# Kernel optimization log

Hardware: AMD Instinct MI355X
Metric: run time of the kernel (lower is better)

Reference implementation:

```python
import jax, jax.numpy as jnp
import numpy as np

B, C, H, W = 8, 64, 112, 112
O, K, PAD, STRIDE = 64, 3, 1, 1
KK = K * K
OH = (H - K + 2 * PAD) // STRIDE + 1
OW = (W - K + 2 * PAD) // STRIDE + 1
L = OH * OW  # number of patches


def setup_inputs() -> dict:
    key = jax.random.key(0)
    k1, k2, k3 = jax.random.split(key, 3)
    x = jax.random.normal(k1, (B, C, H, W), dtype=jnp.float32)
    weight = jax.random.normal(k2, (O, C, K, K), dtype=jnp.float32)
    # one uniformly random kernel position to zero out, per patch (nums=1)
    mask_idx = jax.random.randint(k3, (L,), 0, KK, dtype=jnp.int32)
    return {"x": x, "weight": weight, "mask_idx": mask_idx}


def reference(x, weight, mask_idx):
    b = x.shape[0]
    # im2col: [b, C*KK, OH, OW], feature dim ordered channel-major (c, kh, kw)
    # which matches torch.nn.Unfold ordering.
    patches = jax.lax.conv_general_dilated_patches(
        x, (K, K), (STRIDE, STRIDE), ((PAD, PAD), (PAD, PAD)))
    patches = patches.reshape(b, C * KK, L)  # [b, CK, L]

    # Per-patch mask over kernel positions, tiled across channels
    # (equivalent to mask.repeat(1, in_channels) in the original).
    mask = jnp.ones((L, KK), dtype=x.dtype).at[jnp.arange(L), mask_idx].set(0.0)
    mask_full = jnp.tile(mask, (1, C))  # [L, C*KK]

    # weight.view(O, -1).t() -> [CK, O]; masking the weight rows per patch is
    # mathematically identical to masking the unfolded input per patch, which
    # avoids materializing the [L, CK, O] masked weight tensor.
    w2 = weight.reshape(O, C * KK).T  # [CK, O]
    out = jnp.einsum('bkl,lk,ko->bol', patches, mask_full, w2)  # [b, O, L]
    return out.reshape(b, O, OH, OW)
```

## Files before the change

### kernel.cpp

```cpp
#include <hip/hip_runtime.h>
#include <hip/hip_bf16.h>
#include <cstdint>

#define Bn 8
#define Cn 64
#define Hn 112
#define Wn 112
#define On 64
#define Ln (Hn * Wn)
#define HP 114
#define WP 114

typedef __attribute__((ext_vector_type(4)))  float f32x4;
typedef __attribute__((ext_vector_type(16))) float f32x16;
typedef __attribute__((ext_vector_type(8)))  short bf16x8;
typedef __attribute__((ext_vector_type(4)))  unsigned int u32x4;

__device__ __forceinline__ unsigned f2bf(float f) {
    unsigned u = __float_as_uint(f);
    unsigned r = 0x7fffu + ((u >> 16) & 1u);
    return (u + r) >> 16;
}

__global__ __launch_bounds__(128) void prep_kernel(const float* __restrict__ x,
                                                   const float* __restrict__ w,
                                                   unsigned short* __restrict__ xps,
                                                   unsigned short* __restrict__ wpk) {
    int blk = blockIdx.x;
    int t = threadIdx.x;
    if (blk < 912) {
        int b = blk / HP, row = blk - b * HP;
        int c8  = t >> 4;
        int wpl = t & 15;
        int h = row - 1;
        const float* xb = x + (size_t)b * Cn * Hn * Wn;
        unsigned short* dst = xps + ((size_t)(b * HP + row) * WP) * Cn;
#pragma unroll
        for (int g = 0; g < 8; ++g) {
            int wp = wpl + (g << 4);
            if (wp < WP) {
                int wcol = wp - 1;
                bool inb = ((unsigned)h < (unsigned)Hn) & ((unsigned)wcol < (unsigned)Wn);
                const float* s = xb + ((size_t)(c8 * 8) * Hn + (inb ? h : 0)) * Wn + (inb ? wcol : 0);
                unsigned pk[4];
#pragma unroll
                for (int j = 0; j < 4; ++j) {
                    float v0 = s[(size_t)(2 * j)     * (Hn * Wn)];
                    float v1 = s[(size_t)(2 * j + 1) * (Hn * Wn)];
                    if (!inb) { v0 = 0.f; v1 = 0.f; }
                    pk[j] = f2bf(v0) | (f2bf(v1) << 16);
                }
                u32x4 v; v[0] = pk[0]; v[1] = pk[1]; v[2] = pk[2]; v[3] = pk[3];
                *reinterpret_cast<u32x4*>(dst + (size_t)wp * Cn + c8 * 8) = v;
            }
        }
    } else {
        int idx = (blk - 912) * 2 + (t >> 6);
        int lane = t & 63;
        int kc = idx & 3, wr2 = (idx >> 2) & 1, p = idx >> 3;
        int o  = wr2 * 32 + (lane & 31);
        int cb = kc * 16 + (lane >> 5) * 8;
        unsigned pk[4];
#pragma unroll
        for (int j = 0; j < 4; ++j) {
            float v0 = w[((size_t)o * Cn + cb + 2 * j) * 9 + p];
            float v1 = w[((size_t)o * Cn + cb + 2 * j + 1) * 9 + p];
            pk[j] = f2bf(v0) | (f2bf(v1) << 16);
        }
        u32x4 v; v[0] = pk[0]; v[1] = pk[1]; v[2] = pk[2]; v[3] = pk[3];
        reinterpret_cast<u32x4*>(wpk)[idx * 64 + lane] = v;
    }
}

__global__ __launch_bounds__(256, 4) void conv_direct(const unsigned short* __restrict__ xps,
                                                      const unsigned short* __restrict__ wpk,
                                                      const int* __restrict__ mask_idx,
                                                      float* __restrict__ out) {
    int b  = blockIdx.x & 7;
    int lt = blockIdx.x >> 3;
    int l0 = lt * 128;

    int tid  = threadIdx.x;
    int wave = tid >> 6, lane = tid & 63;
    int hi = lane >> 5;
    int li = lane & 31;

    int lg = l0 + wave * 32 + li;
    int oh = lg / Wn, ow = lg - oh * Wn;
    int mv = mask_idx[lg];

    const char* xb = (const char*)(xps + ((size_t)(b * HP + oh) * WP + ow) * Cn)
                   + hi * 16;

    const u32x4* wv = reinterpret_cast<const u32x4*>(wpk);
    const u32x4 vzero = {0u, 0u, 0u, 0u};

    u32x4 af0[8], af1[8];
#pragma unroll
    for (int f = 0; f < 8; ++f) af0[f] = wv[f * 64 + lane];

    f32x16 acc0 = {}, acc1 = {};

#pragma unroll
    for (int p = 0; p < 9; ++p) {
        u32x4* cur = (p & 1) ? af1 : af0;
        u32x4* nxt = (p & 1) ? af0 : af1;
        if (p < 8) {
#pragma unroll
            for (int f = 0; f < 8; ++f)
                nxt[f] = wv[((p + 1) * 8 + f) * 64 + lane];
        }

        int dh = p / 3, dw = p - dh * 3;
        const char* bp = xb + (dh * WP + dw) * (Cn * 2);
        u32x4 bv[4];
#pragma unroll
        for (int kc = 0; kc < 4; ++kc)
            bv[kc] = *reinterpret_cast<const u32x4*>(bp + kc * 32);
        if (mv == p) { bv[0] = vzero; bv[1] = vzero; bv[2] = vzero; bv[3] = vzero; }

#pragma unroll
        for (int kc = 0; kc < 4; ++kc) {
            bf16x8 bb = *reinterpret_cast<bf16x8*>(&bv[kc]);
            bf16x8 a0 = *reinterpret_cast<bf16x8*>(&cur[kc]);
            bf16x8 a1 = *reinterpret_cast<bf16x8*>(&cur[4 + kc]);
            acc0 = __builtin_amdgcn_mfma_f32_32x32x16_bf16(a0, bb, acc0, 0, 0, 0);
            acc1 = __builtin_amdgcn_mfma_f32_32x32x16_bf16(a1, bb, acc1, 0, 0, 0);
        }
    }

    float* ob = out + (size_t)(b * On) * Ln + lg;
#pragma unroll
    for (int reg = 0; reg < 16; ++reg) {
        int orow = (reg & 3) + 8 * (reg >> 2) + 4 * hi;
        ob[(size_t)orow * Ln]        = acc0[reg];
        ob[(size_t)(orow + 32) * Ln] = acc1[reg];
    }
}

extern "C" void kernel_launch(void* const* d_in, const int* in_sizes, int n_in,
                              void* d_out, int out_size, void* d_ws, size_t ws_size,
                              hipStream_t stream) {
    const float* x    = (const float*)d_in[0];
    const float* w    = (const float*)d_in[1];
    const int*   mask = (const int*)d_in[2];
    float* out = (float*)d_out;

    unsigned short* xps = (unsigned short*)d_ws;
    unsigned short* wpk = (unsigned short*)((char*)d_ws + 13307904);

    prep_kernel<<<948,     128, 0, stream>>>(x, w, xps, wpk);
    conv_direct<<<Bn * 98, 256, 0, stream>>>(xps, wpk, mask, out);
}
```

Measured before the change: 113.3 us.

## Stage padded input rows in LDS with async loads and keep weights in registers

The conv kernel is rebuilt so each 512-thread block handles four output rows of one image. It stages the needed padded input rows into double-buffered LDS with global_load_lds, and the input layout is XOR-swizzled in the prep kernel to avoid bank conflicts. Each wave keeps its 32-output-channel slice of all weights in registers for the whole block. This removes repeated global reads of overlapping 3x3 neighbourhoods and of the weights per tile, at the cost of fewer blocks (224), high register pressure and only a two-stage pipeline.

```diff
diff --git a/kernel.cpp b/kernel.cpp
--- a/kernel.cpp
+++ b/kernel.cpp
@@ -15,6 +15,9 @@
 typedef __attribute__((ext_vector_type(16))) float f32x16;
 typedef __attribute__((ext_vector_type(8)))  short bf16x8;
 typedef __attribute__((ext_vector_type(4)))  unsigned int u32x4;
+
+typedef __attribute__((address_space(3))) unsigned int lds_u32;
+typedef __attribute__((address_space(1))) const unsigned int glob_u32;
 
 __device__ __forceinline__ unsigned f2bf(float f) {
     unsigned u = __float_as_uint(f);
@@ -50,8 +53,9 @@
                     if (!inb) { v0 = 0.f; v1 = 0.f; }
                     pk[j] = f2bf(v0) | (f2bf(v1) << 16);
                 }
+                int slot = c8 ^ (wp & 7);
                 u32x4 v; v[0] = pk[0]; v[1] = pk[1]; v[2] = pk[2]; v[3] = pk[3];
-                *reinterpret_cast<u32x4*>(dst + (size_t)wp * Cn + c8 * 8) = v;
+                *reinterpret_cast<u32x4*>(dst + ((size_t)wp * 8 + slot) * 8) = v;
             }
         }
     } else {
@@ -72,70 +76,110 @@
     }
 }
 
-__global__ __launch_bounds__(256, 4) void conv_direct(const unsigned short* __restrict__ xps,
-                                                      const unsigned short* __restrict__ wpk,
-                                                      const int* __restrict__ mask_idx,
-                                                      float* __restrict__ out) {
+__global__ __launch_bounds__(512, 2) void conv_pipe(const unsigned short* __restrict__ xps,
+                                                    const unsigned short* __restrict__ wpk,
+                                                    const int* __restrict__ mask_idx,
+                                                    float* __restrict__ out) {
+    __shared__ char xs[2][4 * WP * Cn * 2];
+
     int b  = blockIdx.x & 7;
-    int lt = blockIdx.x >> 3;
-    int l0 = lt * 128;
-
+    int rq = blockIdx.x >> 3;
     int tid  = threadIdx.x;
     int wave = tid >> 6, lane = tid & 63;
+    int wr = wave >> 2;
+    int wc = wave & 3;
     int hi = lane >> 5;
     int li = lane & 31;
 
-    int lg = l0 + wave * 32 + li;
-    int oh = lg / Wn, ow = lg - oh * Wn;
-    int mv = mask_idx[lg];
+#define STAGE(TB, OHP) do {                                                        \
+    const char* gsrc_ = (const char*)(xps + ((size_t)(b * HP + (OHP)) * WP) * Cn); \
+    int cb0_ = wave * 456;                                                         \
+    _Pragma("unroll")                                                              \
+    for (int i_ = 0; i_ < 8; ++i_) {                                               \
+        int cb_ = cb0_ + i_ * 64;                                                  \
+        if (i_ < 7 || lane < 8) {                                                  \
+            __builtin_amdgcn_global_load_lds(                                      \
+                (glob_u32*)(gsrc_ + ((size_t)(cb_ + lane) << 4)),                  \
+                reinterpret_cast<lds_u32*>(reinterpret_cast<uintptr_t>(            \
+                    &xs[TB][0] + ((size_t)cb_ << 4))),                             \
+                16, 0, 0);                                                         \
+        }                                                                          \
+    }                                                                              \
+} while (0)
 
-    const char* xb = (const char*)(xps + ((size_t)(b * HP + oh) * WP + ow) * Cn)
-                   + hi * 16;
+    STAGE(0, rq * 4);
 
     const u32x4* wv = reinterpret_cast<const u32x4*>(wpk);
+    u32x4 af[9][4];
+#pragma unroll
+    for (int p = 0; p < 9; ++p)
+#pragma unroll
+        for (int kc = 0; kc < 4; ++kc)
+            af[p][kc] = wv[(p * 8 + wr * 4 + kc) * 64 + lane];
+
+    int mv[2][2], rr[2][2], oww[2][2], lgg[2][2];
+#pragma unroll
+    for (int t = 0; t < 2; ++t)
+#pragma unroll
+        for (int s = 0; s < 2; ++s) {
+            int tl = wc + 4 * s;
+            if (tl < 7) {
+                int idx = tl * 32 + li;
+                int r   = (idx >= Wn) ? 1 : 0;
+                rr[t][s]  = r;
+                oww[t][s] = idx - r * Wn;
+                lgg[t][s] = (rq * 4 + 2 * t) * Wn + idx;
+                mv[t][s]  = mask_idx[lgg[t][s]];
+            }
+        }
+
     const u32x4 vzero = {0u, 0u, 0u, 0u};
 
-    u32x4 af0[8], af1[8];
-#pragma unroll
-    for (int f = 0; f < 8; ++f) af0[f] = wv[f * 64 + lane];
+#define COMPUTE(TB) do {                                                            \
+    _Pragma("unroll")                                                               \
+    for (int s_ = 0; s_ < 2; ++s_) {                                                \
+        if (wc + 4 * s_ < 7) {                                                      \
+            f32x16 acc = {};                                                        \
+            int r0_ = rr[TB][s_], ow0_ = oww[TB][s_], mv0_ = mv[TB][s_];            \
+            _Pragma("unroll")                                                       \
+            for (int p_ = 0; p_ < 9; ++p_) {                                        \
+                int dh_ = p_ / 3, dw_ = p_ - dh_ * 3;                               \
+                int wq_   = ow0_ + dw_;                                             \
+                int base_ = ((r0_ + dh_) * WP + wq_) << 7;                          \
+                int swz_  = (wq_ & 7) << 4;                                         \
+                u32x4 bv[4];                                                        \
+                _Pragma("unroll")                                                   \
+                for (int kc_ = 0; kc_ < 4; ++kc_)                                   \
+                    bv[kc_] = *reinterpret_cast<const u32x4*>(                      \
+                        &xs[TB][0] + ((base_ + ((2 * kc_ + hi) << 4)) ^ swz_));     \
+                if (mv0_ == p_) { bv[0]=vzero; bv[1]=vzero; bv[2]=vzero; bv[3]=vzero; } \
+                _Pragma("unroll")                                                   \
+                for (int kc_ = 0; kc_ < 4; ++kc_) {                                 \
+                    acc = __builtin_amdgcn_mfma_f32_32x32x16_bf16(                  \
+                        *reinterpret_cast<bf16x8*>(&af[p_][kc_]),                   \
+                        *reinterpret_cast<bf16x8*>(&bv[kc_]), acc, 0, 0, 0);        \
+                }                                                                   \
+            }                                                                       \
+            float* ob_ = out + (size_t)(b * On + wr * 32) * Ln + lgg[TB][s_];       \
+            _Pragma("unroll")                                                       \
+            for (int reg_ = 0; reg_ < 16; ++reg_) {                                 \
+                int orow_ = (reg_ & 3) + 8 * (reg_ >> 2) + 4 * hi;                  \
+                ob_[(size_t)orow_ * Ln] = acc[reg_];                                \
+            }                                                                       \
+        }                                                                           \
+    }                                                                               \
+} while (0)
 
-    f32x16 acc0 = {}, acc1 = {};
+    __syncthreads();
 
-#pragma unroll
-    for (int p = 0; p < 9; ++p) {
-        u32x4* cur = (p & 1) ? af1 : af0;
-        u32x4* nxt = (p & 1) ? af0 : af1;
-        if (p < 8) {
-#pragma unroll
-            for (int f = 0; f < 8; ++f)
-                nxt[f] = wv[((p + 1) * 8 + f) * 64 + lane];
-        }
+    STAGE(1, rq * 4 + 2);
+    COMPUTE(0);
 
-        int dh = p / 3, dw = p - dh * 3;
-        const char* bp = xb + (dh * WP + dw) * (Cn * 2);
-        u32x4 bv[4];
-#pragma unroll
-        for (int kc = 0; kc < 4; ++kc)
-            bv[kc] = *reinterpret_cast<const u32x4*>(bp + kc * 32);
-        if (mv == p) { bv[0] = vzero; bv[1] = vzero; bv[2] = vzero; bv[3] = vzero; }
+    __syncthreads();
+    COMPUTE(1);
 
-#pragma unroll
-        for (int kc = 0; kc < 4; ++kc) {
-            bf16x8 bb = *reinterpret_cast<bf16x8*>(&bv[kc]);
-            bf16x8 a0 = *reinterpret_cast<bf16x8*>(&cur[kc]);
-            bf16x8 a1 = *reinterpret_cast<bf16x8*>(&cur[4 + kc]);
-            acc0 = __builtin_amdgcn_mfma_f32_32x32x16_bf16(a0, bb, acc0, 0, 0, 0);
-            acc1 = __builtin_amdgcn_mfma_f32_32x32x16_bf16(a1, bb, acc1, 0, 0, 0);
-        }
-    }
-
-    float* ob = out + (size_t)(b * On) * Ln + lg;
-#pragma unroll
-    for (int reg = 0; reg < 16; ++reg) {
-        int orow = (reg & 3) + 8 * (reg >> 2) + 4 * hi;
-        ob[(size_t)orow * Ln]        = acc0[reg];
-        ob[(size_t)(orow + 32) * Ln] = acc1[reg];
-    }
+#undef STAGE
+#undef COMPUTE
 }
 
 extern "C" void kernel_launch(void* const* d_in, const int* in_sizes, int n_in,
@@ -150,5 +194,5 @@
     unsigned short* wpk = (unsigned short*)((char*)d_ws + 13307904);
 
     prep_kernel<<<948,     128, 0, stream>>>(x, w, xps, wpk);
-    conv_direct<<<Bn * 98, 256, 0, stream>>>(xps, wpk, mask, out);
+    conv_pipe  <<<Bn * 28, 512, 0, stream>>>(xps, wpk, mask, out);
 }
```

Measured after the change: 98.36 us. 13.2% less time.
